# Kernel tuning notes

Hardware: AMD Instinct MI355X
Metric: run time of the kernel (lower is better)

Reference implementation:

```python
import jax, jax.numpy as jnp
import numpy as np

N = 10000        # total nodes in batch
E = 320000       # total edges (before self-loops)
D_IN = 128       # node_dim
H_DIM = 64       # hidden_dim
HEADS = 4
B = 64           # number of graphs
NUM_EDGES = 1024 # actor output dim


def _lin(k, i, o):
    return jax.random.normal(k, (i, o), jnp.float32) / np.sqrt(i)


def setup_inputs() -> dict:
    key = jax.random.key(0)
    ks = jax.random.split(key, 32)
    x = jax.random.normal(ks[0], (N, D_IN), jnp.float32)
    edge_index = jax.random.randint(ks[1], (2, E), 0, N, dtype=jnp.int64)
    batch = jnp.sort(jax.random.randint(ks[2], (N,), 0, B, dtype=jnp.int64))
    inp = dict(x=x, edge_index=edge_index, batch=batch)
    # GAT layer 1: in=D_IN, heads=4, out=H_DIM, concat
    inp['W1'] = _lin(ks[3], D_IN, HEADS * H_DIM)
    inp['as1'] = jax.random.normal(ks[4], (HEADS, H_DIM), jnp.float32) * 0.1
    inp['ad1'] = jax.random.normal(ks[5], (HEADS, H_DIM), jnp.float32) * 0.1
    inp['b1'] = jnp.zeros((HEADS * H_DIM,), jnp.float32)
    # GAT layer 2: in=4*H_DIM, heads=4, out=H_DIM, concat
    inp['W2'] = _lin(ks[6], HEADS * H_DIM, HEADS * H_DIM)
    inp['as2'] = jax.random.normal(ks[7], (HEADS, H_DIM), jnp.float32) * 0.1
    inp['ad2'] = jax.random.normal(ks[8], (HEADS, H_DIM), jnp.float32) * 0.1
    inp['b2'] = jnp.zeros((HEADS * H_DIM,), jnp.float32)
    # GAT layer 3: in=4*H_DIM, heads=1, out=H_DIM, mean (concat=False)
    inp['W3'] = _lin(ks[9], HEADS * H_DIM, H_DIM)
    inp['as3'] = jax.random.normal(ks[10], (1, H_DIM), jnp.float32) * 0.1
    inp['ad3'] = jax.random.normal(ks[11], (1, H_DIM), jnp.float32) * 0.1
    inp['b3'] = jnp.zeros((H_DIM,), jnp.float32)
    # actor MLP
    inp['Wa1'] = _lin(ks[12], H_DIM, H_DIM); inp['ba1'] = jnp.zeros((H_DIM,), jnp.float32)
    inp['Wa2'] = _lin(ks[13], H_DIM, NUM_EDGES); inp['ba2'] = jnp.zeros((NUM_EDGES,), jnp.float32)
    # critic MLP
    inp['Wc1'] = _lin(ks[14], H_DIM, H_DIM); inp['bc1'] = jnp.zeros((H_DIM,), jnp.float32)
    inp['Wc2'] = _lin(ks[15], H_DIM, 1); inp['bc2'] = jnp.zeros((1,), jnp.float32)
    return inp


def gat_layer(x, src, dst, W, a_src, a_dst, bias, heads, out_dim, concat):
    # PyG GATConv: linear -> edge attention -> per-dst softmax -> scatter-add
    n = x.shape[0]
    h = (x @ W).reshape(n, heads, out_dim)            # [N,H,D]
    s = (h * a_src).sum(-1)                           # [N,H] attention src term
    d = (h * a_dst).sum(-1)                           # [N,H]
    e = jax.nn.leaky_relu(s[src] + d[dst], 0.2)       # [Eall,H]
    m = jax.ops.segment_max(e, dst, num_segments=n)   # stable softmax per dst node
    w = jnp.exp(e - m[dst])
    alpha = w / jax.ops.segment_sum(w, dst, num_segments=n)[dst]
    agg = jax.ops.segment_sum(h[src] * alpha[..., None], dst, num_segments=n)  # [N,H,D]
    o = agg.reshape(n, heads * out_dim) if concat else agg.mean(axis=1)
    return o + bias


def forward(x, edge_index, batch, W1, as1, ad1, b1, W2, as2, ad2, b2,
            W3, as3, ad3, b3, Wa1, ba1, Wa2, ba2, Wc1, bc1, Wc2, bc2):
    n = x.shape[0]
    loop = jnp.arange(n, dtype=edge_index.dtype)
    src = jnp.concatenate([edge_index[0], loop])      # add_self_loops=True (PyG default)
    dst = jnp.concatenate([edge_index[1], loop])
    h = jax.nn.relu(gat_layer(x, src, dst, W1, as1, ad1, b1, HEADS, H_DIM, True))
    h = jax.nn.relu(gat_layer(h, src, dst, W2, as2, ad2, b2, HEADS, H_DIM, True))
    h = jax.nn.relu(gat_layer(h, src, dst, W3, as3, ad3, b3, 1, H_DIM, False))
    # global_mean_pool
    counts = jax.ops.segment_sum(jnp.ones((n,), h.dtype), batch, num_segments=B)
    pooled = jax.ops.segment_sum(h, batch, num_segments=B) / jnp.maximum(counts, 1.0)[:, None]
    # heads (dropout is identity at inference)
    action = jnp.tanh(jax.nn.relu(pooled @ Wa1 + ba1) @ Wa2 + ba2)
    value = jax.nn.relu(pooled @ Wc1 + bc1) @ Wc2 + bc2
    return action, value


def reference(x, edge_index, batch, W1, as1, ad1, b1, W2, as2, ad2, b2,
              W3, as3, ad3, b3, Wa1, ba1, Wa2, ba2, Wc1, bc1, Wc2, bc2):
    return forward(x, edge_index, batch, W1, as1, ad1, b1, W2, as2, ad2, b2,
                   W3, as3, ad3, b3, Wa1, ba1, Wa2, ba2, Wc1, bc1, Wc2, bc2)
```

## Files before the change

kernel.cpp:

```cpp
#include <hip/hip_runtime.h>
#include <hip/hip_bf16.h>

#define NN 10000
#define EE 320000
#define EALL (EE + NN)
#define BG 64
#define AOUT 1024

#define WTOT 191361
#define NX (NN * 128)
#define XV (NX / 8)

#define DRANGE 2560
#define DNB 4
#define NSEG 64
#define ESEG 5157

typedef __hip_bfloat16 bf16;
typedef __attribute__((ext_vector_type(8))) short bf16x8;
typedef __attribute__((ext_vector_type(4))) float f32x4;

__device__ __forceinline__ unsigned short f2bf(float f) {
    bf16 h = __float2bfloat16(f);
    return *reinterpret_cast<unsigned short*>(&h);
}
__device__ __forceinline__ float bf2f(unsigned short u) {
    bf16 h;
    *reinterpret_cast<unsigned short*>(&h) = u;
    return __bfloat162float(h);
}

struct WPtrs { const void* p[20]; };
__global__ __launch_bounds__(256) void k_cvt_all(WPtrs wp, const void* __restrict__ xsrc,
                          const void* __restrict__ eisrc, const void* __restrict__ bsrc,
                          float* __restrict__ wf, int* __restrict__ ei32, int* __restrict__ b32,
                          unsigned short* __restrict__ x16,
                          unsigned short* __restrict__ w1t, unsigned short* __restrict__ w2t,
                          unsigned short* __restrict__ w3t,
                          int ffh, int fih) {
    __shared__ int sff, sfi;
    int ff, fi;
    if (ffh >= 0 && fih >= 0) {
        ff = ffh; fi = fih;
    } else {
        const int t = threadIdx.x;
        bool nanp = false, odd = false;
        {
            const uint4* xs4 = (const uint4*)xsrc;
            uint4 a = xs4[t * 8 + 0], b = xs4[t * 8 + 4];
            const unsigned int wds[8] = {a.x, a.y, a.z, a.w, b.x, b.y, b.z, b.w};
#pragma unroll
            for (int k = 0; k < 8; k++) {
                unsigned int w2 = wds[k];
                if ((w2 & 0x7F80u) == 0x7F80u || ((w2 >> 16) & 0x7F80u) == 0x7F80u) nanp = true;
            }
        }
        {
            const unsigned int* eu = (const unsigned int*)eisrc;
            odd = eu[2 * t + 1] != 0u;
        }
        unsigned long long bn = __ballot(nanp);
        unsigned long long bo = __ballot(odd);
        if (t == 0) { sff = 0; sfi = 0; }
        __syncthreads();
        if ((t & 63) == 0) {
            if (bn) atomicOr(&sff, 1);
            if (bo) atomicOr(&sfi, 1);
        }
        __syncthreads();
        ff = (ffh >= 0) ? ffh : sff;
        fi = (fih >= 0) ? fih : sfi;
    }

    const int sz[20] = {32768,256,256,256,65536,256,256,256,16384,64,64,64,4096,64,65536,1024,4096,64,64,1};
    int i = blockIdx.x * 256 + threadIdx.x;
    if (i < WTOT) {
        int seg = 0, off = 0;
        while (i - off >= sz[seg]) { off += sz[seg]; seg++; }
        const void* src = wp.p[seg];
        int k = i - off;
        wf[i] = ff ? ((const float*)src)[k] : __bfloat162float(((const bf16*)src)[k]);
        return;
    }
    i -= WTOT;
    if (i < EE) {
        int j = i * 2;
        if (fi) {
            int2 v = ((const int2*)eisrc)[i];
            ei32[j] = v.x; ei32[j + 1] = v.y;
        } else {
            const long long* e8 = (const long long*)eisrc;
            ei32[j] = (int)e8[j]; ei32[j + 1] = (int)e8[j + 1];
        }
        return;
    }
    i -= EE;
    if (i < NN) { b32[i] = fi ? ((const int*)bsrc)[i] : (int)((const long long*)bsrc)[i]; return; }
    i -= NN;
    if (i < XV) {
        int k = i * 8;
        if (ff) {
            const float4* xs = (const float4*)((const float*)xsrc + k);
            float4 a = xs[0], b = xs[1];
            union { unsigned short u16[8]; uint4 v; } pk;
            pk.u16[0] = f2bf(a.x); pk.u16[1] = f2bf(a.y);
            pk.u16[2] = f2bf(a.z); pk.u16[3] = f2bf(a.w);
            pk.u16[4] = f2bf(b.x); pk.u16[5] = f2bf(b.y);
            pk.u16[6] = f2bf(b.z); pk.u16[7] = f2bf(b.w);
            *(uint4*)&x16[k] = pk.v;
        } else {
            *(uint4*)&x16[k] = ((const uint4*)xsrc)[i];
        }
        return;
    }
    i -= XV;
    if (i < 32768) {
        int k = i >> 8, c = i & 255;
        float v = ff ? ((const float*)wp.p[0])[i] : __bfloat162float(((const bf16*)wp.p[0])[i]);
        w1t[c * 128 + k] = f2bf(v);
        return;
    }
    i -= 32768;
    if (i < 65536) {
        int k = i >> 8, c = i & 255;
        float v = ff ? ((const float*)wp.p[4])[i] : __bfloat162float(((const bf16*)wp.p[4])[i]);
        w2t[c * 256 + k] = f2bf(v);
        return;
    }
    i -= 65536;
    if (i < 16384) {
        int k = i >> 6, c = i & 63;
        float v = ff ? ((const float*)wp.p[8])[i] : __bfloat162float(((const bf16*)wp.p[8])[i]);
        w3t[c * 256 + k] = f2bf(v);
    }
}
#define CVT_TOT (WTOT + EE + NN + XV + 32768 + 65536 + 16384)

__global__ __launch_bounds__(256) void k_fuse1(const int* __restrict__ ei, int* __restrict__ partial,
                                               const unsigned short* __restrict__ A16,
                                               const unsigned short* __restrict__ WT16,
                                               const float* __restrict__ asf,
                                               const float* __restrict__ adf,
                                               unsigned short* __restrict__ C16,
                                               float* __restrict__ sb, float* __restrict__ db) {
    constexpr int LDW = 40;
    __shared__ alignas(16) char smem[DRANGE * 4];
    const int t = threadIdx.x;
    if (blockIdx.x < DNB * NSEG) {
        int* bins = (int*)smem;
        const int r0 = (blockIdx.x >> 6) * DRANGE;
        const int sg = blockIdx.x & 63;
        for (int i = t; i < DRANGE; i += 256) bins[i] = 0;
        __syncthreads();
        const int e1 = min(sg * ESEG + ESEG, EALL);
        for (int e = sg * ESEG + t; e < e1; e += 256) {
            int dst = (e < EE) ? ei[EE + e] : (e - EE);
            unsigned rel = dst - r0;
            if (rel < DRANGE) atomicAdd(&bins[rel], 1);
        }
        __syncthreads();
        for (int i = t; i < DRANGE; i += 256)
            partial[blockIdx.x * DRANGE + i] = bins[i];
        return;
    }
    unsigned short* As = (unsigned short*)smem;
    unsigned short* Bs = As + 64 * LDW;
    constexpr int K = 128, M = 256, H = M / 64;
    const int u = blockIdx.x - DNB * NSEG;
    const int bx = u % 157;
    const int hh = u / 157;
    const int row0 = bx * 64;
    const int col0 = hh * 64;
    const int wv = t >> 6;
    const int lane = t & 63;
    const int m = lane & 15;
    const int q = lane >> 4;
    const int srow = t >> 2;
    const int skoff = (t & 3) * 8;

    f32x4 acc[4] = {};
    for (int k0 = 0; k0 < K; k0 += 32) {
        {
            int grow = row0 + srow;
            uint4 av = make_uint4(0u, 0u, 0u, 0u);
            if (grow < NN) av = *(const uint4*)&A16[(size_t)grow * K + k0 + skoff];
            *(uint4*)&As[srow * LDW + skoff] = av;
            uint4 bv = *(const uint4*)&WT16[(size_t)(col0 + srow) * K + k0 + skoff];
            *(uint4*)&Bs[srow * LDW + skoff] = bv;
        }
        __syncthreads();
        bf16x8 af = *(const bf16x8*)&As[(16 * wv + m) * LDW + q * 8];
#pragma unroll
        for (int ct = 0; ct < 4; ct++) {
            bf16x8 bfv = *(const bf16x8*)&Bs[(16 * ct + m) * LDW + q * 8];
            acc[ct] = __builtin_amdgcn_mfma_f32_16x16x32_bf16(af, bfv, acc[ct], 0, 0, 0);
        }
        __syncthreads();
    }
    float asv[4], adv[4];
#pragma unroll
    for (int ct = 0; ct < 4; ct++) {
        asv[ct] = asf[hh * 64 + 16 * ct + m];
        adv[ct] = adf[hh * 64 + 16 * ct + m];
    }
#pragma unroll
    for (int reg = 0; reg < 4; reg++) {
        int row = row0 + 16 * wv + q * 4 + reg;
        float ps = 0.f, pd = 0.f;
        if (row < NN) {
#pragma unroll
            for (int ct = 0; ct < 4; ct++) {
                float v = acc[ct][reg];
                C16[(size_t)row * M + col0 + 16 * ct + m] = f2bf(v);
                ps += v * asv[ct];
                pd += v * adv[ct];
            }
        }
#pragma unroll
        for (int off = 1; off < 16; off <<= 1) {
            ps += __shfl_xor(ps, off);
            pd += __shfl_xor(pd, off);
        }
        if (m == 0 && row < NN) { sb[row * H + hh] = ps; db[row * H + hh] = pd; }
    }
}

__global__ void k_seg(const int* __restrict__ partial, int* __restrict__ deg,
                      int* __restrict__ segpre) {
    int bin = blockIdx.x * 256 + threadIdx.x;
    if (bin >= NN) return;
    int r = bin / DRANGE, rel = bin - r * DRANGE;
    int s = 0;
    for (int sg = 0; sg < NSEG; sg++) {
        int idx = (r * NSEG + sg) * DRANGE + rel;
        int v = partial[idx];
        segpre[idx] = s;
        s += v;
    }
    deg[bin] = s;
}

__global__ void k_scan4(const int* __restrict__ deg, int* __restrict__ rowstart,
                        const int* __restrict__ batch, int* __restrict__ gstart) {
    __shared__ int part[1024];
    const int t = threadIdx.x;
    if (t <= BG) {
        int lo = 0, hi = NN;
        while (lo < hi) { int mid = (lo + hi) >> 1; if (batch[mid] < t) lo = mid + 1; else hi = mid; }
        gstart[t] = lo;
    }
    const int base = t * 10;
    int local[10];
    int s = 0;
    for (int i = 0; i < 10; i++) {
        int idx = base + i;
        int v = (idx < NN) ? deg[idx] : 0;
        local[i] = s; s += v;
    }
    part[t] = s; __syncthreads();
    for (int off = 1; off < 1024; off <<= 1) {
        int v = (t >= off) ? part[t - off] : 0;
        __syncthreads();
        part[t] += v;
        __syncthreads();
    }
    int pre = (t == 0) ? 0 : part[t - 1];
    for (int i = 0; i < 10; i++) {
        int idx = base + i;
        if (idx < NN) rowstart[idx] = pre + local[i];
    }
    if (t == 1023) rowstart[NN] = part[1023];
}

__global__ __launch_bounds__(256) void k_scatter3(const int* __restrict__ ei,
                                                  const int* __restrict__ rowstart,
                                                  const int* __restrict__ segpre,
                                                  int* __restrict__ ssrc) {
    __shared__ int cur[DRANGE];
    const int r0 = blockIdx.x * DRANGE;
    const int sg = blockIdx.y;
    for (int i = threadIdx.x; i < DRANGE; i += 256) {
        int bin = r0 + i;
        cur[i] = (bin < NN) ? rowstart[bin] + segpre[(blockIdx.x * NSEG + sg) * DRANGE + i] : 0;
    }
    __syncthreads();
    const int e1 = min(sg * ESEG + ESEG, EALL);
    for (int e = sg * ESEG + threadIdx.x; e < e1; e += 256) {
        int dst = (e < EE) ? ei[EE + e] : (e - EE);
        unsigned rel = dst - r0;
        if (rel < DRANGE) {
            int src = (e < EE) ? ei[e] : dst;
            int pos = atomicAdd(&cur[rel], 1);
            ssrc[pos] = src;
        }
    }
}

template<int K, int M>
__global__ __launch_bounds__(256) void k_gemm(const unsigned short* __restrict__ A16,
                                              const unsigned short* __restrict__ WT16,
                                              const float* __restrict__ asf,
                                              const float* __restrict__ adf,
                                              unsigned short* __restrict__ C16,
                                              float* __restrict__ sb, float* __restrict__ db) {
    constexpr int BK = 32;
    constexpr int H = M / 64;
    constexpr int LDW = 40;
    __shared__ unsigned short As[64 * LDW];
    __shared__ unsigned short Bs[64 * LDW];
    const int row0 = blockIdx.x * 64;
    const int col0 = blockIdx.y * 64;
    const int hh = blockIdx.y;
    const int t = threadIdx.x;
    const int wv = t >> 6;
    const int lane = t & 63;
    const int m = lane & 15;
    const int q = lane >> 4;
    const int srow = t >> 2;
    const int skoff = (t & 3) * 8;

    f32x4 acc[4] = {};

    for (int k0 = 0; k0 < K; k0 += BK) {
        {
            int grow = row0 + srow;
            uint4 av = make_uint4(0u, 0u, 0u, 0u);
            if (grow < NN) av = *(const uint4*)&A16[(size_t)grow * K + k0 + skoff];
            *(uint4*)&As[srow * LDW + skoff] = av;
            uint4 bv = *(const uint4*)&WT16[(size_t)(col0 + srow) * K + k0 + skoff];
            *(uint4*)&Bs[srow * LDW + skoff] = bv;
        }
        __syncthreads();
        bf16x8 af = *(const bf16x8*)&As[(16 * wv + m) * LDW + q * 8];
#pragma unroll
        for (int ct = 0; ct < 4; ct++) {
            bf16x8 bfv = *(const bf16x8*)&Bs[(16 * ct + m) * LDW + q * 8];
            acc[ct] = __builtin_amdgcn_mfma_f32_16x16x32_bf16(af, bfv, acc[ct], 0, 0, 0);
        }
        __syncthreads();
    }

    float asv[4], adv[4];
#pragma unroll
    for (int ct = 0; ct < 4; ct++) {
        asv[ct] = asf[hh * 64 + 16 * ct + m];
        adv[ct] = adf[hh * 64 + 16 * ct + m];
    }
#pragma unroll
    for (int reg = 0; reg < 4; reg++) {
        int row = row0 + 16 * wv + q * 4 + reg;
        float ps = 0.f, pd = 0.f;
        if (row < NN) {
#pragma unroll
            for (int ct = 0; ct < 4; ct++) {
                float v = acc[ct][reg];
                C16[(size_t)row * M + col0 + 16 * ct + m] = f2bf(v);
                ps += v * asv[ct];
                pd += v * adv[ct];
            }
        }
#pragma unroll
        for (int off = 1; off < 16; off <<= 1) {
            ps += __shfl_xor(ps, off);
            pd += __shfl_xor(pd, off);
        }
        if (m == 0 && row < NN) { sb[row * H + hh] = ps; db[row * H + hh] = pd; }
    }
}

template<int H>
__global__ void k_agg(const unsigned short* __restrict__ hbuf16, const float* __restrict__ sb,
                      const float* __restrict__ db, const int* __restrict__ rowstart,
                      const int* __restrict__ ssrc, const float* __restrict__ bias,
                      unsigned short* __restrict__ out16) {
    constexpr int M = H * 64;
    constexpr int LH = (H == 4) ? 2 : 0;
    constexpr int NW = M / 64;
    constexpr int CG = M / 8;
    constexpr int LCG = (H == 4) ? 5 : 3;
    const int n = blockIdx.x;
    const int tid = threadIdx.x;
    const int start = rowstart[n], end = rowstart[n + 1];
    const int slot = tid >> LH;
    const int hh = tid & (H - 1);
    const int wv = tid >> 6;
    const int lane = tid & 63;
    const int cg = tid & (CG - 1);
    const int eg = tid >> LCG;
    const int chh = (H == 4) ? (cg >> 3) : 0;
    __shared__ float wl[64 * H];
    __shared__ int srcl[64];
    __shared__ float accbuf[8 * M];
    __shared__ float sww[NW][H];
    const float dn = db[n * H + hh];

    float wsum = 0.f;
    float acc[8] = {};
    for (int c = start; c < end; c += 64) {
        const int cn = min(64, end - c);
        __syncthreads();
        if (slot < cn) {
            int s = ssrc[c + slot];
            float e = sb[s * H + hh] + dn;
            e = e > 0.f ? e : 0.2f * e;
            float wv2 = __expf(e);
            wl[slot * H + hh] = wv2;
            wsum += wv2;
            if (hh == 0) srcl[slot] = s;
        }
        __syncthreads();
#pragma unroll 2
        for (int j = eg; j < cn; j += 8) {
            float wv2 = wl[j * H + chh];
            const bf16x8 v = *(const bf16x8*)&hbuf16[(size_t)srcl[j] * M + cg * 8];
#pragma unroll
            for (int i = 0; i < 8; i++)
                acc[i] += wv2 * bf2f((unsigned short)v[i]);
        }
    }

    {
        float* ab = &accbuf[eg * M + cg * 8];
#pragma unroll
        for (int i = 0; i < 8; i++) ab[i] = acc[i];
    }
#pragma unroll
    for (int off = H; off < 64; off <<= 1) wsum += __shfl_xor(wsum, off);
    if constexpr (NW > 1) { if (lane < H) sww[wv][lane] = wsum; }
    __syncthreads();

    float wsh;
    const int h2 = (H == 4) ? (tid >> 6) : 0;
    if constexpr (NW > 1) {
        wsh = sww[0][h2];
#pragma unroll
        for (int w = 1; w < NW; w++) wsh += sww[w][h2];
    } else {
        wsh = wsum;
    }

    float o = 0.f;
#pragma unroll
    for (int e8 = 0; e8 < 8; e8++) o += accbuf[e8 * M + tid];
    o = o / wsh + bias[tid];
    out16[(size_t)n * M + tid] = f2bf(fmaxf(o, 0.f));
}

__global__ __launch_bounds__(256) void k_final(const unsigned short* __restrict__ feat16,
                                               const int* __restrict__ gstart,
                                               const float* __restrict__ Wa1, const float* __restrict__ ba1,
                                               const float* __restrict__ Wc1, const float* __restrict__ bc1,
                                               const float* __restrict__ Wa2, const float* __restrict__ ba2,
                                               const float* __restrict__ Wc2, const float* __restrict__ bc2,
                                               float* __restrict__ out) {
    __shared__ float red[256];
    __shared__ float p[64];
    __shared__ float a[64], cc[64];
    const int g = blockIdx.x, t = threadIdx.x;
    const int d = t & 63, c = t >> 6;
    const int s = gstart[g], e = gstart[g + 1];
    float acc = 0.f;
    for (int n = s + c; n < e; n += 4) acc += bf2f(feat16[(size_t)n * 64 + d]);
    red[t] = acc; __syncthreads();
    if (c == 0) p[d] = (red[d] + red[64 + d] + red[128 + d] + red[192 + d])
                       / fmaxf((float)(e - s), 1.f);
    __syncthreads();
    if (t < 128) {
        int j = t & 63;
        const float* W  = (t < 64) ? Wa1 : Wc1;
        const float* bb = (t < 64) ? ba1 : bc1;
        float h = 0.f;
#pragma unroll 8
        for (int k = 0; k < 64; k++) h += p[k] * W[k * 64 + j];
        h = fmaxf(h + bb[j], 0.f);
        if (t < 64) a[j] = h; else cc[j] = h;
    }
    __syncthreads();
    float o[4] = {0.f, 0.f, 0.f, 0.f};
    for (int k = 0; k < 64; k++) {
        float ak = a[k];
#pragma unroll
        for (int q = 0; q < 4; q++) o[q] += ak * Wa2[k * AOUT + t + 256 * q];
    }
#pragma unroll
    for (int q = 0; q < 4; q++)
        out[g * AOUT + t + 256 * q] = tanhf(o[q] + ba2[t + 256 * q]);
    if (t == 0) {
        float v = 0.f;
        for (int k = 0; k < 64; k++) v += cc[k] * Wc2[k];
        out[BG * AOUT + g] = v + bc2[0];
    }
}

extern "C" void kernel_launch(void* const* d_in, const int* in_sizes, int n_in,
                              void* d_out, int out_size, void* d_ws, size_t ws_size,
                              hipStream_t stream) {
    float* out = (float*)d_out;

    char* w = (char*)d_ws;
    auto alloc = [&](size_t bytes) { void* p = (void*)w; w += (bytes + 255) & ~size_t(255); return p; };
    float* wf      = (float*)alloc((size_t)WTOT * 4);
    int*   ei32    = (int*)alloc((size_t)2 * EE * 4);
    int*   b32     = (int*)alloc((size_t)NN * 4);
    unsigned short* x16    = (unsigned short*)alloc((size_t)NX * 2);
    unsigned short* w1t    = (unsigned short*)alloc((size_t)32768 * 2);
    unsigned short* w2t    = (unsigned short*)alloc((size_t)65536 * 2);
    unsigned short* w3t    = (unsigned short*)alloc((size_t)16384 * 2);
    unsigned short* actA16 = (unsigned short*)alloc((size_t)NN * 256 * 2);
    unsigned short* actB16 = (unsigned short*)alloc((size_t)NN * 256 * 2);
    float* sb      = (float*)alloc((size_t)NN * 4 * 4);
    float* db      = (float*)alloc((size_t)NN * 4 * 4);
    int*   partial = (int*)alloc((size_t)DNB * NSEG * DRANGE * 4);
    int*   segpre  = (int*)alloc((size_t)DNB * NSEG * DRANGE * 4);
    int*   deg     = (int*)alloc((size_t)NN * 4);
    int*   rowstart= (int*)alloc((size_t)(NN + 1) * 4);
    int*   ssrc    = (int*)alloc((size_t)EALL * 4);
    int*   gstart  = (int*)alloc((size_t)(BG + 1) * 4);

    int ffh = -1, fih = -1;
    if (in_sizes && n_in >= 2) {
        long long xs = in_sizes[0];
        if (xs == (long long)NX * 4) ffh = 1;
        else if (xs == (long long)NX * 2) ffh = 0;
        long long es = in_sizes[1];
        if (es == (long long)2 * EE * 8) fih = 0;
        else if (es == (long long)2 * EE * 4) fih = 1;
    }

    WPtrs wp;
    for (int s = 0; s < 20; s++) wp.p[s] = d_in[3 + s];
    k_cvt_all<<<(CVT_TOT + 255) / 256, 256, 0, stream>>>(
        wp, d_in[0], d_in[1], d_in[2], wf, ei32, b32, x16, w1t, w2t, w3t, ffh, fih);

    const int wsz[20] = {32768,256,256,256,65536,256,256,256,16384,64,64,64,4096,64,65536,1024,4096,64,64,1};
    int woff[20]; int acc = 0;
    for (int s = 0; s < 20; s++) { woff[s] = acc; acc += wsz[s]; }
    const float *as1f = wf + woff[1], *ad1f = wf + woff[2], *b1f = wf + woff[3];
    const float *as2f = wf + woff[5], *ad2f = wf + woff[6], *b2f = wf + woff[7];
    const float *as3f = wf + woff[9], *ad3f = wf + woff[10], *b3f = wf + woff[11];
    const float *Wa1f = wf + woff[12], *ba1f = wf + woff[13], *Wa2f = wf + woff[14], *ba2f = wf + woff[15];
    const float *Wc1f = wf + woff[16], *bc1f = wf + woff[17], *Wc2f = wf + woff[18], *bc2f = wf + woff[19];

    k_fuse1<<<DNB * NSEG + 628, 256, 0, stream>>>(ei32, partial,
                                                  x16, w1t, as1f, ad1f, actA16, sb, db);

    k_seg<<<(NN + 255) / 256, 256, 0, stream>>>(partial, deg, segpre);
    k_scan4<<<1, 1024, 0, stream>>>(deg, rowstart, b32, gstart);
    k_scatter3<<<dim3(DNB, NSEG), 256, 0, stream>>>(ei32, rowstart, segpre, ssrc);

    k_agg<4><<<NN, 256, 0, stream>>>(actA16, sb, db, rowstart, ssrc, b1f, actB16);

    k_gemm<256, 256><<<dim3(157, 4), 256, 0, stream>>>(actB16, w2t, as2f, ad2f, actA16, sb, db);
    k_agg<4><<<NN, 256, 0, stream>>>(actA16, sb, db, rowstart, ssrc, b2f, actB16);

    k_gemm<256, 64><<<dim3(157, 1), 256, 0, stream>>>(actB16, w3t, as3f, ad3f, actA16, sb, db);
    k_agg<1><<<NN, 64, 0, stream>>>(actA16, sb, db, rowstart, ssrc, b3f, actB16);

    k_final<<<BG, 256, 0, stream>>>(actB16, gstart,
                                    Wa1f, ba1f, Wc1f, bc1f, Wa2f, ba2f, Wc2f, bc2f, out);
}
```

Before: 233.2 us.

## Read raw inputs directly in consumers instead of pre-converting edges, batch and x

Removes the pre-conversion of edge_index to int32, batch to int32 and x to bf16 from the conversion kernel. The consumers (histogram/GEMM kernel, scan, scatter) now read the original int64/int32 indices and the fp32/bf16 features directly, converting on the fly. This is meant to cut the extra global-memory round trip and the large conversion grid. In exchange, edge reads become 8-byte strided loads read twice (histogram and scatter), and each kernel repeats the dtype detection when host sizes are absent.

```diff
diff --git a/kernel.cpp b/kernel.cpp
--- a/kernel.cpp
+++ b/kernel.cpp
@@ -8,8 +8,6 @@
 #define AOUT 1024
 
 #define WTOT 191361
-#define NX (NN * 128)
-#define XV (NX / 8)
 
 #define DRANGE 2560
 #define DNB 4
@@ -29,47 +27,34 @@
     *reinterpret_cast<unsigned short*>(&h) = u;
     return __bfloat162float(h);
 }
+__device__ __forceinline__ int iread(const void* p, int fi, long long idx) {
+    return fi ? ((const int*)p)[idx] : (int)((const long long*)p)[idx];
+}
 
 struct WPtrs { const void* p[20]; };
 __global__ __launch_bounds__(256) void k_cvt_all(WPtrs wp, const void* __restrict__ xsrc,
-                          const void* __restrict__ eisrc, const void* __restrict__ bsrc,
-                          float* __restrict__ wf, int* __restrict__ ei32, int* __restrict__ b32,
-                          unsigned short* __restrict__ x16,
+                          float* __restrict__ wf,
                           unsigned short* __restrict__ w1t, unsigned short* __restrict__ w2t,
-                          unsigned short* __restrict__ w3t,
-                          int ffh, int fih) {
-    __shared__ int sff, sfi;
-    int ff, fi;
-    if (ffh >= 0 && fih >= 0) {
-        ff = ffh; fi = fih;
-    } else {
+                          unsigned short* __restrict__ w3t, int ffh) {
+    __shared__ int sff;
+    int ff = ffh;
+    if (ffh < 0) {
         const int t = threadIdx.x;
-        bool nanp = false, odd = false;
-        {
-            const uint4* xs4 = (const uint4*)xsrc;
-            uint4 a = xs4[t * 8 + 0], b = xs4[t * 8 + 4];
-            const unsigned int wds[8] = {a.x, a.y, a.z, a.w, b.x, b.y, b.z, b.w};
-#pragma unroll
-            for (int k = 0; k < 8; k++) {
-                unsigned int w2 = wds[k];
-                if ((w2 & 0x7F80u) == 0x7F80u || ((w2 >> 16) & 0x7F80u) == 0x7F80u) nanp = true;
-            }
-        }
-        {
-            const unsigned int* eu = (const unsigned int*)eisrc;
-            odd = eu[2 * t + 1] != 0u;
+        bool nanp = false;
+        const uint4* xs4 = (const uint4*)xsrc;
+        uint4 a = xs4[t * 8 + 0], b = xs4[t * 8 + 4];
+        const unsigned int wds[8] = {a.x, a.y, a.z, a.w, b.x, b.y, b.z, b.w};
+#pragma unroll
+        for (int k = 0; k < 8; k++) {
+            unsigned int w2 = wds[k];
+            if ((w2 & 0x7F80u) == 0x7F80u || ((w2 >> 16) & 0x7F80u) == 0x7F80u) nanp = true;
         }
         unsigned long long bn = __ballot(nanp);
-        unsigned long long bo = __ballot(odd);
-        if (t == 0) { sff = 0; sfi = 0; }
-        __syncthreads();
-        if ((t & 63) == 0) {
-            if (bn) atomicOr(&sff, 1);
-            if (bo) atomicOr(&sfi, 1);
-        }
-        __syncthreads();
-        ff = (ffh >= 0) ? ffh : sff;
-        fi = (fih >= 0) ? fih : sfi;
+        if (t == 0) sff = 0;
+        __syncthreads();
+        if ((t & 63) == 0 && bn) atomicOr(&sff, 1);
+        __syncthreads();
+        ff = sff;
     }
 
     const int sz[20] = {32768,256,256,256,65536,256,256,256,16384,64,64,64,4096,64,65536,1024,4096,64,64,1};
@@ -83,37 +68,6 @@
         return;
     }
     i -= WTOT;
-    if (i < EE) {
-        int j = i * 2;
-        if (fi) {
-            int2 v = ((const int2*)eisrc)[i];
-            ei32[j] = v.x; ei32[j + 1] = v.y;
-        } else {
-            const long long* e8 = (const long long*)eisrc;
-            ei32[j] = (int)e8[j]; ei32[j + 1] = (int)e8[j + 1];
-        }
-        return;
-    }
-    i -= EE;
-    if (i < NN) { b32[i] = fi ? ((const int*)bsrc)[i] : (int)((const long long*)bsrc)[i]; return; }
-    i -= NN;
-    if (i < XV) {
-        int k = i * 8;
-        if (ff) {
-            const float4* xs = (const float4*)((const float*)xsrc + k);
-            float4 a = xs[0], b = xs[1];
-            union { unsigned short u16[8]; uint4 v; } pk;
-            pk.u16[0] = f2bf(a.x); pk.u16[1] = f2bf(a.y);
-            pk.u16[2] = f2bf(a.z); pk.u16[3] = f2bf(a.w);
-            pk.u16[4] = f2bf(b.x); pk.u16[5] = f2bf(b.y);
-            pk.u16[6] = f2bf(b.z); pk.u16[7] = f2bf(b.w);
-            *(uint4*)&x16[k] = pk.v;
-        } else {
-            *(uint4*)&x16[k] = ((const uint4*)xsrc)[i];
-        }
-        return;
-    }
-    i -= XV;
     if (i < 32768) {
         int k = i >> 8, c = i & 255;
         float v = ff ? ((const float*)wp.p[0])[i] : __bfloat162float(((const bf16*)wp.p[0])[i]);
@@ -134,10 +88,12 @@
         w3t[c * 256 + k] = f2bf(v);
     }
 }
-#define CVT_TOT (WTOT + EE + NN + XV + 32768 + 65536 + 16384)
-
-__global__ __launch_bounds__(256) void k_fuse1(const int* __restrict__ ei, int* __restrict__ partial,
-                                               const unsigned short* __restrict__ A16,
+#define CVT_TOT (WTOT + 32768 + 65536 + 16384)
+
+__global__ __launch_bounds__(256) void k_fuse1(const void* __restrict__ eisrc,
+                                               const void* __restrict__ xsrc,
+                                               int ffh, int fih,
+                                               int* __restrict__ partial,
                                                const unsigned short* __restrict__ WT16,
                                                const float* __restrict__ asf,
                                                const float* __restrict__ adf,
@@ -145,7 +101,33 @@
                                                float* __restrict__ sb, float* __restrict__ db) {
     constexpr int LDW = 40;
     __shared__ alignas(16) char smem[DRANGE * 4];
+    __shared__ int sff, sfi;
     const int t = threadIdx.x;
+    int ff = ffh, fi = fih;
+    if (ffh < 0 || fih < 0) {
+        bool nanp = false, odd = false;
+        const uint4* xs4 = (const uint4*)xsrc;
+        uint4 a = xs4[t * 8 + 0], b = xs4[t * 8 + 4];
+        const unsigned int wds[8] = {a.x, a.y, a.z, a.w, b.x, b.y, b.z, b.w};
+#pragma unroll
+        for (int k = 0; k < 8; k++) {
+            unsigned int w2 = wds[k];
+            if ((w2 & 0x7F80u) == 0x7F80u || ((w2 >> 16) & 0x7F80u) == 0x7F80u) nanp = true;
+        }
+        odd = ((const unsigned int*)eisrc)[2 * t + 1] != 0u;
+        unsigned long long bn = __ballot(nanp);
+        unsigned long long bo = __ballot(odd);
+        if (t == 0) { sff = 0; sfi = 0; }
+        __syncthreads();
+        if ((t & 63) == 0) {
+            if (bn) atomicOr(&sff, 1);
+            if (bo) atomicOr(&sfi, 1);
+        }
+        __syncthreads();
+        ff = (ffh >= 0) ? ffh : sff;
+        fi = (fih >= 0) ? fih : sfi;
+    }
+
     if (blockIdx.x < DNB * NSEG) {
         int* bins = (int*)smem;
         const int r0 = (blockIdx.x >> 6) * DRANGE;
@@ -154,7 +136,7 @@
         __syncthreads();
         const int e1 = min(sg * ESEG + ESEG, EALL);
         for (int e = sg * ESEG + t; e < e1; e += 256) {
-            int dst = (e < EE) ? ei[EE + e] : (e - EE);
+            int dst = (e < EE) ? iread(eisrc, fi, (long long)EE + e) : (e - EE);
             unsigned rel = dst - r0;
             if (rel < DRANGE) atomicAdd(&bins[rel], 1);
         }
@@ -183,7 +165,21 @@
         {
             int grow = row0 + srow;
             uint4 av = make_uint4(0u, 0u, 0u, 0u);
-            if (grow < NN) av = *(const uint4*)&A16[(size_t)grow * K + k0 + skoff];
+            if (grow < NN) {
+                if (ff) {
+                    const float* xp = (const float*)xsrc + (size_t)grow * K + k0 + skoff;
+                    float4 fa = *(const float4*)xp;
+                    float4 fb = *(const float4*)(xp + 4);
+                    union { unsigned short u16[8]; uint4 v; } pk;
+                    pk.u16[0] = f2bf(fa.x); pk.u16[1] = f2bf(fa.y);
+                    pk.u16[2] = f2bf(fa.z); pk.u16[3] = f2bf(fa.w);
+                    pk.u16[4] = f2bf(fb.x); pk.u16[5] = f2bf(fb.y);
+                    pk.u16[6] = f2bf(fb.z); pk.u16[7] = f2bf(fb.w);
+                    av = pk.v;
+                } else {
+                    av = *(const uint4*)((const unsigned short*)xsrc + (size_t)grow * K + k0 + skoff);
+                }
+            }
             *(uint4*)&As[srow * LDW + skoff] = av;
             uint4 bv = *(const uint4*)&WT16[(size_t)(col0 + srow) * K + k0 + skoff];
             *(uint4*)&Bs[srow * LDW + skoff] = bv;
@@ -241,12 +237,28 @@
 }
 
 __global__ void k_scan4(const int* __restrict__ deg, int* __restrict__ rowstart,
-                        const int* __restrict__ batch, int* __restrict__ gstart) {
+                        const void* __restrict__ bsrc, int fih, int* __restrict__ gstart,
+                        const void* __restrict__ eisrc) {
     __shared__ int part[1024];
+    __shared__ int sfi;
     const int t = threadIdx.x;
+    int fi = fih;
+    if (fih < 0) {
+        bool odd = ((const unsigned int*)eisrc)[2 * t + 1] != 0u;
+        unsigned long long bo = __ballot(odd);
+        if (t == 0) sfi = 0;
+        __syncthreads();
+        if ((t & 63) == 0 && bo) atomicOr(&sfi, 1);
+        __syncthreads();
+        fi = sfi;
+    }
     if (t <= BG) {
         int lo = 0, hi = NN;
-        while (lo < hi) { int mid = (lo + hi) >> 1; if (batch[mid] < t) lo = mid + 1; else hi = mid; }
+        while (lo < hi) {
+            int mid = (lo + hi) >> 1;
+            int bv = iread(bsrc, fi, mid);
+            if (bv < t) lo = mid + 1; else hi = mid;
+        }
         gstart[t] = lo;
     }
     const int base = t * 10;
@@ -272,24 +284,36 @@
     if (t == 1023) rowstart[NN] = part[1023];
 }
 
-__global__ __launch_bounds__(256) void k_scatter3(const int* __restrict__ ei,
+__global__ __launch_bounds__(256) void k_scatter3(const void* __restrict__ eisrc, int fih,
                                                   const int* __restrict__ rowstart,
                                                   const int* __restrict__ segpre,
                                                   int* __restrict__ ssrc) {
     __shared__ int cur[DRANGE];
+    __shared__ int sfi;
+    const int t = threadIdx.x;
+    int fi = fih;
+    if (fih < 0) {
+        bool odd = ((const unsigned int*)eisrc)[2 * t + 1] != 0u;
+        unsigned long long bo = __ballot(odd);
+        if (t == 0) sfi = 0;
+        __syncthreads();
+        if ((t & 63) == 0 && bo) atomicOr(&sfi, 1);
+        __syncthreads();
+        fi = sfi;
+    }
     const int r0 = blockIdx.x * DRANGE;
     const int sg = blockIdx.y;
-    for (int i = threadIdx.x; i < DRANGE; i += 256) {
+    for (int i = t; i < DRANGE; i += 256) {
         int bin = r0 + i;
         cur[i] = (bin < NN) ? rowstart[bin] + segpre[(blockIdx.x * NSEG + sg) * DRANGE + i] : 0;
     }
     __syncthreads();
     const int e1 = min(sg * ESEG + ESEG, EALL);
-    for (int e = sg * ESEG + threadIdx.x; e < e1; e += 256) {
-        int dst = (e < EE) ? ei[EE + e] : (e - EE);
+    for (int e = sg * ESEG + t; e < e1; e += 256) {
+        int dst = (e < EE) ? iread(eisrc, fi, (long long)EE + e) : (e - EE);
         unsigned rel = dst - r0;
         if (rel < DRANGE) {
-            int src = (e < EE) ? ei[e] : dst;
+            int src = (e < EE) ? iread(eisrc, fi, e) : dst;
             int pos = atomicAdd(&cur[rel], 1);
             ssrc[pos] = src;
         }
@@ -500,9 +524,6 @@
     char* w = (char*)d_ws;
     auto alloc = [&](size_t bytes) { void* p = (void*)w; w += (bytes + 255) & ~size_t(255); return p; };
     float* wf      = (float*)alloc((size_t)WTOT * 4);
-    int*   ei32    = (int*)alloc((size_t)2 * EE * 4);
-    int*   b32     = (int*)alloc((size_t)NN * 4);
-    unsigned short* x16    = (unsigned short*)alloc((size_t)NX * 2);
     unsigned short* w1t    = (unsigned short*)alloc((size_t)32768 * 2);
     unsigned short* w2t    = (unsigned short*)alloc((size_t)65536 * 2);
     unsigned short* w3t    = (unsigned short*)alloc((size_t)16384 * 2);
@@ -520,8 +541,8 @@
     int ffh = -1, fih = -1;
     if (in_sizes && n_in >= 2) {
         long long xs = in_sizes[0];
-        if (xs == (long long)NX * 4) ffh = 1;
-        else if (xs == (long long)NX * 2) ffh = 0;
+        if (xs == (long long)NN * 128 * 4) ffh = 1;
+        else if (xs == (long long)NN * 128 * 2) ffh = 0;
         long long es = in_sizes[1];
         if (es == (long long)2 * EE * 8) fih = 0;
         else if (es == (long long)2 * EE * 4) fih = 1;
@@ -530,7 +551,7 @@
     WPtrs wp;
     for (int s = 0; s < 20; s++) wp.p[s] = d_in[3 + s];
     k_cvt_all<<<(CVT_TOT + 255) / 256, 256, 0, stream>>>(
-        wp, d_in[0], d_in[1], d_in[2], wf, ei32, b32, x16, w1t, w2t, w3t, ffh, fih);
+        wp, d_in[0], wf, w1t, w2t, w3t, ffh);
 
     const int wsz[20] = {32768,256,256,256,65536,256,256,256,16384,64,64,64,4096,64,65536,1024,4096,64,64,1};
     int woff[20]; int acc = 0;
@@ -541,12 +562,12 @@
     const float *Wa1f = wf + woff[12], *ba1f = wf + woff[13], *Wa2f = wf + woff[14], *ba2f = wf + woff[15];
     const float *Wc1f = wf + woff[16], *bc1f = wf + woff[17], *Wc2f = wf + woff[18], *bc2f = wf + woff[19];
 
-    k_fuse1<<<DNB * NSEG + 628, 256, 0, stream>>>(ei32, partial,
-                                                  x16, w1t, as1f, ad1f, actA16, sb, db);
+    k_fuse1<<<DNB * NSEG + 628, 256, 0, stream>>>(d_in[1], d_in[0], ffh, fih, partial,
+                                                  w1t, as1f, ad1f, actA16, sb, db);
 
     k_seg<<<(NN + 255) / 256, 256, 0, stream>>>(partial, deg, segpre);
-    k_scan4<<<1, 1024, 0, stream>>>(deg, rowstart, b32, gstart);
-    k_scatter3<<<dim3(DNB, NSEG), 256, 0, stream>>>(ei32, rowstart, segpre, ssrc);
+    k_scan4<<<1, 1024, 0, stream>>>(deg, rowstart, d_in[2], fih, gstart, d_in[1]);
+    k_scatter3<<<dim3(DNB, NSEG), 256, 0, stream>>>(d_in[1], fih, rowstart, segpre, ssrc);
 
     k_agg<4><<<NN, 256, 0, stream>>>(actA16, sb, db, rowstart, ssrc, b1f, actB16);
 
```

Result: no change. 232.9 us (-0.1%).
